# Optimization experiments

Measured on AMD Instinct MI355X. Metric: run time of the kernel, lower is better.

The kernel has to match this reference:

```python
import jax, jax.numpy as jnp
import numpy as np

SEQ_LEN = 4096
D_MODEL = 1024


def _positional_encoding(seq_len, d_model, dtype=jnp.float32):
    pos = jnp.arange(seq_len, dtype=jnp.float32)[:, None]            # [S, 1]
    even = jnp.arange(0, d_model, 2, dtype=jnp.float32)              # [D/2]
    denom = jnp.power(10000.0, even / d_model)                       # [D/2]
    angle = pos / denom                                              # [S, D/2]
    # interleave sin (even dims) and cos (odd dims)
    pe = jnp.stack([jnp.sin(angle), jnp.cos(angle)], axis=-1)        # [S, D/2, 2]
    return pe.reshape(seq_len, d_model).astype(dtype)                # [S, D]


def setup_inputs() -> dict:
    key = jax.random.key(0)
    x = jax.random.normal(key, (8, SEQ_LEN, D_MODEL), dtype=jnp.float32)
    return {"input": x}


def reference(input) -> jnp.ndarray:
    pe = _positional_encoding(input.shape[-2], input.shape[-1], input.dtype)
    return input + pe
```

## Files before the change

### kernel.cpp

```cpp
#include <hip/hip_runtime.h>
#include <hip/hip_bf16.h>


#define SEQ_LEN 4096
#define D_MODEL 1024

using f32x4 = __attribute__((ext_vector_type(4))) float;

__global__ void __launch_bounds__(256)
pe_add_kernel(const float* __restrict__ in, float* __restrict__ out) {
    constexpr int D4 = D_MODEL / 4;

    int idx = blockIdx.x * blockDim.x + threadIdx.x;

    const f32x4* src = reinterpret_cast<const f32x4*>(in)  + idx;
    f32x4 v = *src;

    int d4 = idx & (D4 - 1);
    int s  = (idx >> 8) & (SEQ_LEN - 1);

    constexpr float K = -0.025952563241307517f;
    float sf   = (float)s;
    int   p0   = d4 * 2;
    float ang0 = sf * exp2f((float)p0 * K);
    float ang1 = sf * exp2f((float)(p0 + 1) * K);
    float s0, c0, s1, c1;
    sincosf(ang0, &s0, &c0);
    sincosf(ang1, &s1, &c1);

    v.x += s0; v.y += c0; v.z += s1; v.w += c1;
    __builtin_nontemporal_store(v, reinterpret_cast<f32x4*>(out) + idx);
}

extern "C" void kernel_launch(void* const* d_in, const int* in_sizes, int n_in,
                              void* d_out, int out_size, void* d_ws, size_t ws_size,
                              hipStream_t stream) {
    const float* in  = (const float*)d_in[0];
    float*       out = (float*)d_out;

    int total4 = in_sizes[0] / 4;
    dim3 block(256);
    dim3 grid(total4 / 256);
    pe_add_kernel<<<grid, block, 0, stream>>>(in, out);
}
```

Before: 221.1 us.

## Precompute positional-encoding table once, then stream-add it across batches

Splits the work into a kernel that builds a 16 MB sin/cos table in workspace and a second kernel that adds the table to each batch, using nontemporal loads for the input. This removes the transcendental math being recomputed for every batch element, at the cost of an extra launch, 16 MB of table writes and 16 MB of table reads per batch, which the cache may absorb. If the workspace is too small, it falls back to the original fused kernel.

Measured after the change: 225.3 us. About the same (+1.9%).

```diff
diff --git a/kernel.cpp b/kernel.cpp
--- a/kernel.cpp
+++ b/kernel.cpp
@@ -8,16 +8,11 @@
 using f32x4 = __attribute__((ext_vector_type(4))) float;
 
 __global__ void __launch_bounds__(256)
-pe_add_kernel(const float* __restrict__ in, float* __restrict__ out) {
+pe_table_kernel(float* __restrict__ pe) {
     constexpr int D4 = D_MODEL / 4;
-
     int idx = blockIdx.x * blockDim.x + threadIdx.x;
-
-    const f32x4* src = reinterpret_cast<const f32x4*>(in)  + idx;
-    f32x4 v = *src;
-
-    int d4 = idx & (D4 - 1);
-    int s  = (idx >> 8) & (SEQ_LEN - 1);
+    int d4  = idx & (D4 - 1);
+    int s   = idx >> 8;
 
     constexpr float K = -0.025952563241307517f;
     float sf   = (float)s;
@@ -28,6 +23,39 @@
     sincosf(ang0, &s0, &c0);
     sincosf(ang1, &s1, &c1);
 
+    reinterpret_cast<f32x4*>(pe)[idx] = f32x4{s0, c0, s1, c1};
+}
+
+__global__ void __launch_bounds__(256)
+pe_add_kernel(const float* __restrict__ in, const float* __restrict__ pe,
+              float* __restrict__ out) {
+    constexpr int PLANE4 = SEQ_LEN * (D_MODEL / 4);
+
+    int idx = blockIdx.x * blockDim.x + threadIdx.x;
+
+    f32x4 v = __builtin_nontemporal_load(
+                  reinterpret_cast<const f32x4*>(in) + idx);
+    f32x4 p = reinterpret_cast<const f32x4*>(pe)[idx & (PLANE4 - 1)];
+
+    v.x += p.x; v.y += p.y; v.z += p.z; v.w += p.w;
+    __builtin_nontemporal_store(v, reinterpret_cast<f32x4*>(out) + idx);
+}
+
+__global__ void __launch_bounds__(256)
+pe_add_fused_kernel(const float* __restrict__ in, float* __restrict__ out) {
+    constexpr int D4 = D_MODEL / 4;
+    int idx = blockIdx.x * blockDim.x + threadIdx.x;
+    f32x4 v = *(reinterpret_cast<const f32x4*>(in) + idx);
+    int d4 = idx & (D4 - 1);
+    int s  = (idx >> 8) & (SEQ_LEN - 1);
+    constexpr float K = -0.025952563241307517f;
+    float sf = (float)s;
+    int p0 = d4 * 2;
+    float ang0 = sf * exp2f((float)p0 * K);
+    float ang1 = sf * exp2f((float)(p0 + 1) * K);
+    float s0, c0, s1, c1;
+    sincosf(ang0, &s0, &c0);
+    sincosf(ang1, &s1, &c1);
     v.x += s0; v.y += c0; v.z += s1; v.w += c1;
     __builtin_nontemporal_store(v, reinterpret_cast<f32x4*>(out) + idx);
 }
@@ -38,8 +66,15 @@
     const float* in  = (const float*)d_in[0];
     float*       out = (float*)d_out;
 
+    constexpr size_t PE_BYTES = (size_t)SEQ_LEN * D_MODEL * sizeof(float);
     int total4 = in_sizes[0] / 4;
-    dim3 block(256);
-    dim3 grid(total4 / 256);
-    pe_add_kernel<<<grid, block, 0, stream>>>(in, out);
+
+    if (ws_size >= PE_BYTES) {
+        float* pe = (float*)d_ws;
+        constexpr int T1 = SEQ_LEN * (D_MODEL / 4);
+        pe_table_kernel<<<T1 / 256, 256, 0, stream>>>(pe);
+        pe_add_kernel<<<total4 / 256, 256, 0, stream>>>(in, pe, out);
+    } else {
+        pe_add_fused_kernel<<<total4 / 256, 256, 0, stream>>>(in, out);
+    }
 }
```
